# Performance work log

Hardware: AMD Instinct MI355X
Metric: run time of the kernel (lower is better)

The kernel has to match this reference:

```python
import jax, jax.numpy as jnp
import numpy as np

D_MODEL = 1024
D_STATE = 128
D_CONV = 4
EXPAND = 2
HEADDIM = 64
D_INNER = EXPAND * D_MODEL          # 2048
NHEADS = D_INNER // HEADDIM         # 32
NGROUPS = 1
CONV_DIM = D_INNER + 2 * NGROUPS * D_STATE            # 2304
D_IN_PROJ = 2 * D_INNER + 2 * NGROUPS * D_STATE + NHEADS  # 4384
NUM_CLASS = 48
BATCH = 2
SEQLEN = 512


def setup_inputs() -> dict:
    key = jax.random.key(0)
    ks = jax.random.split(key, 8)
    s = 0.02
    inputs = jax.random.normal(ks[0], (BATCH, SEQLEN, D_MODEL), jnp.float32)
    W_in = jax.random.normal(ks[1], (D_MODEL, D_IN_PROJ), jnp.float32) * s
    conv_w = jax.random.normal(ks[2], (CONV_DIM, D_CONV), jnp.float32) * 0.2
    conv_b = jnp.zeros((CONV_DIM,), jnp.float32)
    # dt_bias = inverse-softplus of dt sampled in [1e-3, 0.1] (mamba init)
    dt = jnp.exp(jax.random.uniform(ks[3], (NHEADS,), jnp.float32) * (np.log(0.1) - np.log(1e-3)) + np.log(1e-3))
    dt_bias = dt + jnp.log(-jnp.expm1(-dt))
    A_log = jnp.log(jax.random.uniform(ks[4], (NHEADS,), jnp.float32, 1.0, 16.0))
    D = jnp.ones((NHEADS,), jnp.float32)
    norm_w = jnp.ones((D_INNER,), jnp.float32)
    W_out = jax.random.normal(ks[5], (D_INNER, D_MODEL), jnp.float32) * s
    W_cls = jax.random.normal(ks[6], (D_INNER, NUM_CLASS), jnp.float32) * s
    b_cls = jnp.zeros((NUM_CLASS,), jnp.float32)
    return {"inputs": inputs, "W_in": W_in, "conv_w": conv_w, "conv_b": conv_b,
            "dt_bias": dt_bias, "A_log": A_log, "D": D, "norm_w": norm_w,
            "W_out": W_out, "W_cls": W_cls, "b_cls": b_cls}


def _forward(inputs, W_in, conv_w, conv_b, dt_bias, A_log, D, norm_w, W_out, W_cls, b_cls):
    B, L, _ = inputs.shape
    zxbcdt = inputs @ W_in                                     # (B,L,4384)
    z, xBC, dt = jnp.split(zxbcdt, [D_INNER, D_INNER + CONV_DIM], axis=-1)
    dt = jax.nn.softplus(dt + dt_bias)                         # (B,L,H)
    # causal depthwise conv over time on (x,B,C)
    xBC_t = jnp.pad(jnp.transpose(xBC, (0, 2, 1)), ((0, 0), (0, 0), (D_CONV - 1, 0)))
    xBC_c = jax.lax.conv_general_dilated(xBC_t, conv_w[:, None, :], (1,), 'VALID',
                                         feature_group_count=CONV_DIM)
    xBC = jax.nn.silu(jnp.transpose(xBC_c, (0, 2, 1)) + conv_b)
    x, Bm, Cm = jnp.split(xBC, [D_INNER, D_INNER + D_STATE], axis=-1)
    x = x.reshape(B, L, NHEADS, HEADDIM)
    A = -jnp.exp(A_log)                                        # (H,)
    dA = jnp.exp(dt * A)                                       # (B,L,H)

    def step(state, inp):
        # state: (B,H,P,N) -- selective SSM recurrence (chunk_size=1 path)
        x_t, B_t, C_t, dt_t, dA_t = inp
        state = state * dA_t[:, :, None, None] + jnp.einsum('bhp,bn,bh->bhpn', x_t, B_t, dt_t)
        y_t = jnp.einsum('bhpn,bn->bhp', state, C_t)
        return state, y_t

    state0 = jnp.zeros((B, NHEADS, HEADDIM, D_STATE), inputs.dtype)
    xs = (jnp.transpose(x, (1, 0, 2, 3)), jnp.transpose(Bm, (1, 0, 2)),
          jnp.transpose(Cm, (1, 0, 2)), jnp.transpose(dt, (1, 0, 2)),
          jnp.transpose(dA, (1, 0, 2)))
    _, ys = jax.lax.scan(step, state0, xs)                     # ys: (L,B,H,P)
    y = jnp.transpose(ys, (1, 0, 2, 3)) + D[None, None, :, None] * x
    y = y.reshape(B, L, D_INNER)
    # gated RMSNorm: rmsnorm(y * silu(z)) * weight
    y = y * jax.nn.silu(z)
    y = y * jax.lax.rsqrt(jnp.mean(y * y, axis=-1, keepdims=True) + 1e-5) * norm_w
    # hidden_states (d_inner=2048) go through the per-timestep classifier
    preds = y @ W_cls + b_cls                                  # (B,L,num_class)
    return preds


def reference(inputs, W_in, conv_w, conv_b, dt_bias, A_log, D, norm_w, W_out, W_cls, b_cls):
    return _forward(inputs, W_in, conv_w, conv_b, dt_bias, A_log, D, norm_w, W_out, W_cls, b_cls)
```

## Files before the change

kernel.cpp:

```cpp
#include <hip/hip_runtime.h>
#include <hip/hip_bf16.h>
#include <cstdint>

#define BATCH 2
#define SEQLEN 512
#define BL (BATCH*SEQLEN)
#define DMODEL 1024
#define DINNER 2048
#define NHEADS 32
#define HEADDIM 64
#define DSTATE 128
#define CONVDIM 2304
#define DINPROJ 4384
#define NPROJPAD 4480
#define NCLS 48
#define QC 64
#define NCH 8

typedef short bf16x8 __attribute__((ext_vector_type(8)));
typedef float f32x4  __attribute__((ext_vector_type(4)));
typedef unsigned int u32;
typedef const __attribute__((address_space(1))) u32 gu32;
typedef __attribute__((address_space(3))) u32 lu32;

static __device__ __forceinline__ void gl16(const void* g, void* l) {
    __builtin_amdgcn_global_load_lds((gu32*)g, (lu32*)l, 16, 0, 0);
}

static __device__ __forceinline__ unsigned short f2bf(float f) {
    unsigned u = __float_as_uint(f);
    unsigned r = (u + 0x7FFFu + ((u >> 16) & 1u)) >> 16;
    return (unsigned short)r;
}
static __device__ __forceinline__ float bf2f(unsigned short u) {
    return __uint_as_float(((unsigned)u) << 16);
}

__global__ __launch_bounds__(256) void k_prep(const float* __restrict__ in,
                                              unsigned short* __restrict__ abf,
                                              const float* __restrict__ W,
                                              unsigned short* __restrict__ Wt,
                                              const float* __restrict__ Wcls,
                                              unsigned short* __restrict__ Wtc) {
    __shared__ float tile[32][33];
    int bid = blockIdx.x;
    int tid = threadIdx.x;
    if (bid < 1024) {
        int i = (bid * 256 + tid) * 4;
        float4 v = *(const float4*)(in + i);
        ushort4 o;
        o.x = f2bf(v.x); o.y = f2bf(v.y); o.z = f2bf(v.z); o.w = f2bf(v.w);
        *(ushort4*)(abf + i) = o;
    } else if (bid < 1024 + 4384) {
        int t = bid - 1024;
        int n0 = (t % 137) * 32;
        int k0 = (t / 137) * 32;
        int tx = tid & 31, ty = tid >> 5;
#pragma unroll
        for (int i = 0; i < 4; ++i) {
            int k = k0 + ty + i * 8;
            tile[ty + i * 8][tx] = W[(size_t)k * DINPROJ + n0 + tx];
        }
        __syncthreads();
#pragma unroll
        for (int i = 0; i < 4; ++i) {
            int n = n0 + ty + i * 8;
            Wt[(size_t)n * DMODEL + k0 + tx] = f2bf(tile[tx][ty + i * 8]);
        }
    } else {
        int n = bid - (1024 + 4384);
        for (int k = tid; k < DINNER; k += 256)
            Wtc[(size_t)n * DINNER + k] = f2bf(Wcls[(size_t)k * NCLS + n]);
    }
}

__global__ __launch_bounds__(256) void k_gemm_in(const unsigned short* __restrict__ A,
                                                 const unsigned short* __restrict__ Bt,
                                                 unsigned short* __restrict__ C) {
    __shared__ unsigned short As[2 * 4096];
    __shared__ unsigned short Bs[2 * 5120];
    const int tid  = threadIdx.x;
    const int m0   = blockIdx.y * 128;
    const int n0   = blockIdx.x * 160;
    const int w    = tid >> 6;
    const int lane = tid & 63;
    const int wm   = w >> 1, wn = w & 1;
    const int fr   = lane & 15, fq = lane >> 4;
    const int lrow = lane >> 2;
    const int skg  = (lane & 3) * 8;
    const unsigned short* gA0 = A + (size_t)(m0 + w * 16 + lrow) * DMODEL + skg;
    const unsigned short* gA1 = gA0 + (size_t)64 * DMODEL;

    f32x4 acc[4][5] = {};
    for (int k0 = 0; k0 < DMODEL; k0 += 64) {
        __syncthreads();
#pragma unroll
        for (int hh = 0; hh < 2; ++hh) {
            int kg = k0 + hh * 32;
            gl16(gA0 + kg, As + hh * 4096 + w * 512);
            gl16(gA1 + kg, As + hh * 4096 + 2048 + w * 512);
            for (int o = w; o < 10; o += 4) {
                const unsigned short* gB = Bt + (size_t)(n0 + o * 16 + lrow) * DMODEL + skg + kg;
                gl16(gB, Bs + hh * 5120 + o * 512);
            }
        }
        __syncthreads();
#pragma unroll
        for (int hh = 0; hh < 2; ++hh) {
            bf16x8 af[4], bfr[5];
#pragma unroll
            for (int mt = 0; mt < 4; ++mt)
                af[mt] = *(const bf16x8*)(&As[hh * 4096 + (wm * 64 + mt * 16 + fr) * 32 + fq * 8]);
#pragma unroll
            for (int nt = 0; nt < 5; ++nt)
                bfr[nt] = *(const bf16x8*)(&Bs[hh * 5120 + (wn * 80 + nt * 16 + fr) * 32 + fq * 8]);
#pragma unroll
            for (int mt = 0; mt < 4; ++mt)
#pragma unroll
                for (int nt = 0; nt < 5; ++nt)
                    acc[mt][nt] = __builtin_amdgcn_mfma_f32_16x16x32_bf16(af[mt], bfr[nt], acc[mt][nt], 0, 0, 0);
        }
    }
#pragma unroll
    for (int mt = 0; mt < 4; ++mt) {
#pragma unroll
        for (int nt = 0; nt < 5; ++nt) {
            int col = n0 + wn * 80 + nt * 16 + fr;
            if (col < DINPROJ) {
#pragma unroll
                for (int r = 0; r < 4; ++r) {
                    int row = m0 + wm * 64 + mt * 16 + fq * 4 + r;
                    C[(size_t)row * DINPROJ + col] = f2bf(acc[mt][nt][r]);
                }
            }
        }
    }
}

__global__ __launch_bounds__(256) void k_conv_dt(const unsigned short* __restrict__ zx,
                                                 const float* __restrict__ conv_w,
                                                 const float* __restrict__ conv_b,
                                                 const float* __restrict__ dt_bias,
                                                 float* __restrict__ xbc,
                                                 float* __restrict__ dtb) {
    int row = blockIdx.y;
    int c   = blockIdx.x * 256 + threadIdx.x;
    int b = row >> 9, l = row & 511;
    if (c < CONVDIM) {
        float acc = conv_b[c];
#pragma unroll
        for (int j = 0; j < 4; ++j) {
            int ls = l - 3 + j;
            float v = (ls >= 0) ? bf2f(zx[((size_t)(b * SEQLEN + ls)) * DINPROJ + DINNER + c]) : 0.f;
            acc += v * conv_w[c * 4 + j];
        }
        float s = acc / (1.f + expf(-acc));
        xbc[(size_t)row * CONVDIM + c] = s;
    } else if (c < CONVDIM + NHEADS) {
        int h = c - CONVDIM;
        float raw = bf2f(zx[(size_t)row * DINPROJ + (DINNER + CONVDIM) + h]) + dt_bias[h];
        float dt = (raw > 20.f) ? raw : log1pf(expf(raw));
        dtb[row * NHEADS + h] = dt;
    }
}

__global__ __launch_bounds__(256) void k_chunk(const float* __restrict__ xbc,
                                               const float* __restrict__ dtb,
                                               const float* __restrict__ A_log,
                                               const float* __restrict__ Dvec,
                                               unsigned short* __restrict__ yb,
                                               unsigned short* __restrict__ Sc_bf,
                                               float* __restrict__ lam_g,
                                               float* __restrict__ esc_g) {
    const int gid = blockIdx.x;
    const int cq = gid & 7;
    const int h = (gid >> 3) & 31;
    const int b = gid >> 8;
    const int row0 = b * SEQLEN + cq * QC;

    __shared__ float cumS[QC], wS[QC], dtS[QC];
    __shared__ unsigned short Xt[QC][72];
    __shared__ unsigned short Bs[QC][136];
    __shared__ unsigned short BtW[DSTATE][72];
    __shared__ unsigned short Cs[QC][136];
    __shared__ unsigned short Gs[QC][72];

    const int tid = threadIdx.x;
    if (tid < 64) {
        float dtv = dtb[(size_t)(row0 + tid) * NHEADS + h];
        float nA = -expf(A_log[h]);
        float x = dtv * nA;
#pragma unroll
        for (int off = 1; off < 64; off <<= 1) {
            float v = __shfl_up(x, off, 64);
            if (tid >= off) x += v;
        }
        float cumTot = __shfl(x, 63, 64);
        cumS[tid] = x;
        dtS[tid] = dtv;
        wS[tid] = expf(cumTot - x) * dtv;
        esc_g[(size_t)gid * QC + tid] = expf(x);
        if (tid == 0) lam_g[gid] = expf(cumTot);
    }
    __syncthreads();

    {
        int row = tid >> 2;
        int g = tid & 3;
        const float* rp = xbc + (size_t)(row0 + row) * CONVDIM;
        float wrow = wS[row];
#pragma unroll
        for (int i = 0; i < 4; ++i) {
            float4 v = *(const float4*)(rp + h * HEADDIM + g * 16 + i * 4);
            int p = g * 16 + i * 4;
            Xt[p + 0][row] = f2bf(v.x);
            Xt[p + 1][row] = f2bf(v.y);
            Xt[p + 2][row] = f2bf(v.z);
            Xt[p + 3][row] = f2bf(v.w);
        }
#pragma unroll
        for (int i = 0; i < 8; ++i) {
            int n = g * 32 + i * 4;
            float4 v = *(const float4*)(rp + DINNER + n);
            ushort4 u;
            u.x = f2bf(v.x); u.y = f2bf(v.y); u.z = f2bf(v.z); u.w = f2bf(v.w);
            *(ushort4*)(&Bs[row][n]) = u;
            BtW[n + 0][row] = f2bf(v.x * wrow);
            BtW[n + 1][row] = f2bf(v.y * wrow);
            BtW[n + 2][row] = f2bf(v.z * wrow);
            BtW[n + 3][row] = f2bf(v.w * wrow);
        }
#pragma unroll
        for (int i = 0; i < 8; ++i) {
            int n = g * 32 + i * 4;
            float4 v = *(const float4*)(rp + DINNER + DSTATE + n);
            ushort4 u;
            u.x = f2bf(v.x); u.y = f2bf(v.y); u.z = f2bf(v.z); u.w = f2bf(v.w);
            *(ushort4*)(&Cs[row][n]) = u;
        }
    }
    __syncthreads();

    const int w = tid >> 6, lane = tid & 63;
    const int fr = lane & 15, fq = lane >> 4, fk = (lane >> 4) * 8;

    f32x4 accG[4] = {};
#pragma unroll
    for (int kk = 0; kk < 4; ++kk) {
        bf16x8 a = *(const bf16x8*)(&Cs[w * 16 + fr][kk * 32 + fk]);
#pragma unroll
        for (int nt = 0; nt < 4; ++nt) {
            bf16x8 bb = *(const bf16x8*)(&Bs[nt * 16 + fr][kk * 32 + fk]);
            accG[nt] = __builtin_amdgcn_mfma_f32_16x16x32_bf16(a, bb, accG[nt], 0, 0, 0);
        }
    }
#pragma unroll
    for (int nt = 0; nt < 4; ++nt) {
        int s = nt * 16 + fr;
        float cs = cumS[s], dts = dtS[s];
#pragma unroll
        for (int r = 0; r < 4; ++r) {
            int t = w * 16 + fq * 4 + r;
            float val = (s <= t) ? accG[nt][r] * expf(cumS[t] - cs) * dts : 0.f;
            Gs[t][s] = f2bf(val);
        }
    }
    __syncthreads();

    f32x4 accY[4] = {};
#pragma unroll
    for (int kk = 0; kk < 2; ++kk) {
        bf16x8 a = *(const bf16x8*)(&Gs[w * 16 + fr][kk * 32 + fk]);
#pragma unroll
        for (int pt = 0; pt < 4; ++pt) {
            bf16x8 bb = *(const bf16x8*)(&Xt[pt * 16 + fr][kk * 32 + fk]);
            accY[pt] = __builtin_amdgcn_mfma_f32_16x16x32_bf16(a, bb, accY[pt], 0, 0, 0);
        }
    }
    f32x4 accS[8] = {};
#pragma unroll
    for (int kk = 0; kk < 2; ++kk) {
        bf16x8 a = *(const bf16x8*)(&Xt[w * 16 + fr][kk * 32 + fk]);
#pragma unroll
        for (int nt = 0; nt < 8; ++nt) {
            bf16x8 bb = *(const bf16x8*)(&BtW[nt * 16 + fr][kk * 32 + fk]);
            accS[nt] = __builtin_amdgcn_mfma_f32_16x16x32_bf16(a, bb, accS[nt], 0, 0, 0);
        }
    }
    float Dh = Dvec[h];
#pragma unroll
    for (int pt = 0; pt < 4; ++pt) {
        int p = pt * 16 + fr;
#pragma unroll
        for (int r = 0; r < 4; ++r) {
            int t = w * 16 + fq * 4 + r;
            float xv = bf2f(Xt[p][t]);
            yb[(size_t)(row0 + t) * DINNER + h * HEADDIM + p] = f2bf(accY[pt][r] + Dh * xv);
        }
    }
    unsigned short* scp = Sc_bf + (size_t)gid * (HEADDIM * DSTATE);
#pragma unroll
    for (int nt = 0; nt < 8; ++nt) {
        int n = nt * 16 + fr;
#pragma unroll
        for (int r = 0; r < 4; ++r) {
            int p = w * 16 + fq * 4 + r;
            scp[p * DSTATE + n] = f2bf(accS[nt][r]);
        }
    }
}

__global__ __launch_bounds__(256) void k_cross(const float* __restrict__ xbc,
                                               const float* __restrict__ esc_g,
                                               const unsigned short* __restrict__ Sc_bf,
                                               const float* __restrict__ lam_g,
                                               unsigned short* __restrict__ yb) {
    const int gid = blockIdx.x;
    const int cq = gid & 7;
    if (cq == 0) return;
    const int h = (gid >> 3) & 31;
    const int b = gid >> 8;
    const int row0 = b * SEQLEN + cq * QC;
    __shared__ unsigned short Ct[QC][136];
    __shared__ unsigned short Ss[QC][136];
    const int tid = threadIdx.x;
    const int gbase = gid & ~7;

    float coef[NCH - 1];
    {
        float prod = 1.f;
        for (int c2 = cq - 1; c2 >= 0; --c2) {
            coef[c2] = prod;
            prod *= lam_g[gbase + c2];
        }
    }
    {
        int row = tid >> 2, g = tid & 3;
        const float* rp = xbc + (size_t)(row0 + row) * CONVDIM + DINNER + DSTATE;
        float esc = esc_g[(size_t)gid * QC + row];
#pragma unroll
        for (int i = 0; i < 8; ++i) {
            int n = g * 32 + i * 4;
            float4 v = *(const float4*)(rp + n);
            ushort4 u;
            u.x = f2bf(v.x * esc); u.y = f2bf(v.y * esc);
            u.z = f2bf(v.z * esc); u.w = f2bf(v.w * esc);
            *(ushort4*)(&Ct[row][n]) = u;
        }
        float acc32[32];
#pragma unroll
        for (int i = 0; i < 32; ++i) acc32[i] = 0.f;
        for (int c2 = 0; c2 < cq; ++c2) {
            const unsigned short* sp = Sc_bf + (size_t)(gbase + c2) * (HEADDIM * DSTATE)
                                     + row * DSTATE + g * 32;
            float cf = coef[c2];
#pragma unroll
            for (int i = 0; i < 8; ++i) {
                ushort4 v = *(const ushort4*)(sp + i * 4);
                acc32[i * 4 + 0] += cf * bf2f(v.x);
                acc32[i * 4 + 1] += cf * bf2f(v.y);
                acc32[i * 4 + 2] += cf * bf2f(v.z);
                acc32[i * 4 + 3] += cf * bf2f(v.w);
            }
        }
#pragma unroll
        for (int i = 0; i < 8; ++i) {
            ushort4 u;
            u.x = f2bf(acc32[i * 4 + 0]);
            u.y = f2bf(acc32[i * 4 + 1]);
            u.z = f2bf(acc32[i * 4 + 2]);
            u.w = f2bf(acc32[i * 4 + 3]);
            *(ushort4*)(&Ss[row][g * 32 + i * 4]) = u;
        }
    }
    __syncthreads();
    const int w = tid >> 6, lane = tid & 63;
    const int fr = lane & 15, fq = lane >> 4, fk = (lane >> 4) * 8;
    f32x4 acc[4] = {};
#pragma unroll
    for (int kk = 0; kk < 4; ++kk) {
        bf16x8 a = *(const bf16x8*)(&Ct[w * 16 + fr][kk * 32 + fk]);
#pragma unroll
        for (int pt = 0; pt < 4; ++pt) {
            bf16x8 bb = *(const bf16x8*)(&Ss[pt * 16 + fr][kk * 32 + fk]);
            acc[pt] = __builtin_amdgcn_mfma_f32_16x16x32_bf16(a, bb, acc[pt], 0, 0, 0);
        }
    }
#pragma unroll
    for (int pt = 0; pt < 4; ++pt) {
        int p = pt * 16 + fr;
#pragma unroll
        for (int r = 0; r < 4; ++r) {
            int t = w * 16 + fq * 4 + r;
            size_t yi = (size_t)(row0 + t) * DINNER + h * HEADDIM + p;
            yb[yi] = f2bf(bf2f(yb[yi]) + acc[pt][r]);
        }
    }
}

__global__ __launch_bounds__(256) void k_gn_cls(const unsigned short* __restrict__ zx,
                                                const unsigned short* __restrict__ yb,
                                                const float* __restrict__ nw,
                                                const unsigned short* __restrict__ Wt,
                                                const float* __restrict__ bcls,
                                                float* __restrict__ out) {
    __shared__ unsigned short Gs[16][2048];
    __shared__ float scaleS[16];
    __shared__ float Rs[3][4][256];
    const int m0 = blockIdx.x * 16;
    const int tid = threadIdx.x;
    const int w = tid >> 6, lane = tid & 63;

#pragma unroll
    for (int i = 0; i < 4; ++i) {
        int rl = w * 4 + i;
        int row = m0 + rl;
        const unsigned short* yr = yb + (size_t)row * DINNER;
        const unsigned short* zr = zx + (size_t)row * DINPROJ;
        float gv[32];
        float ss = 0.f;
#pragma unroll
        for (int i2 = 0; i2 < 4; ++i2) {
            int k = i2 * 512 + lane * 8;
            ushort4 ya = *(const ushort4*)(yr + k);
            ushort4 ybq = *(const ushort4*)(yr + k + 4);
            ushort4 za = *(const ushort4*)(zr + k);
            ushort4 zbq = *(const ushort4*)(zr + k + 4);
            float ys[8] = {bf2f(ya.x), bf2f(ya.y), bf2f(ya.z), bf2f(ya.w),
                           bf2f(ybq.x), bf2f(ybq.y), bf2f(ybq.z), bf2f(ybq.w)};
            float zs[8] = {bf2f(za.x), bf2f(za.y), bf2f(za.z), bf2f(za.w),
                           bf2f(zbq.x), bf2f(zbq.y), bf2f(zbq.z), bf2f(zbq.w)};
#pragma unroll
            for (int j = 0; j < 8; ++j) {
                float sil = zs[j] / (1.f + expf(-zs[j]));
                float gg = ys[j] * sil;
                gv[i2 * 8 + j] = gg;
                ss += gg * gg;
            }
        }
#pragma unroll
        for (int off = 32; off >= 1; off >>= 1) ss += __shfl_xor(ss, off, 64);
        if (lane == 0) scaleS[rl] = rsqrtf(ss / (float)DINNER + 1e-5f);
#pragma unroll
        for (int i2 = 0; i2 < 4; ++i2) {
            int k = i2 * 512 + lane * 8;
            ushort4 u0, u1;
            u0.x = f2bf(gv[i2 * 8 + 0]); u0.y = f2bf(gv[i2 * 8 + 1]);
            u0.z = f2bf(gv[i2 * 8 + 2]); u0.w = f2bf(gv[i2 * 8 + 3]);
            u1.x = f2bf(gv[i2 * 8 + 4]); u1.y = f2bf(gv[i2 * 8 + 5]);
            u1.z = f2bf(gv[i2 * 8 + 6]); u1.w = f2bf(gv[i2 * 8 + 7]);
            *(ushort4*)(&Gs[rl][k]) = u0;
            *(ushort4*)(&Gs[rl][k + 4]) = u1;
        }
    }
    __syncthreads();
    {
        int k0 = tid * 8;
        float4 n0 = *(const float4*)(nw + k0);
        float4 n1 = *(const float4*)(nw + k0 + 4);
        float nv[8] = {n0.x, n0.y, n0.z, n0.w, n1.x, n1.y, n1.z, n1.w};
#pragma unroll
        for (int r = 0; r < 16; ++r) {
            float sc = scaleS[r];
            ushort4 a0 = *(const ushort4*)(&Gs[r][k0]);
            ushort4 a1 = *(const ushort4*)(&Gs[r][k0 + 4]);
            ushort4 o0, o1;
            o0.x = f2bf(bf2f(a0.x) * sc * nv[0]); o0.y = f2bf(bf2f(a0.y) * sc * nv[1]);
            o0.z = f2bf(bf2f(a0.z) * sc * nv[2]); o0.w = f2bf(bf2f(a0.w) * sc * nv[3]);
            o1.x = f2bf(bf2f(a1.x) * sc * nv[4]); o1.y = f2bf(bf2f(a1.y) * sc * nv[5]);
            o1.z = f2bf(bf2f(a1.z) * sc * nv[6]); o1.w = f2bf(bf2f(a1.w) * sc * nv[7]);
            *(ushort4*)(&Gs[r][k0]) = o0;
            *(ushort4*)(&Gs[r][k0 + 4]) = o1;
        }
    }
    __syncthreads();
    const int fr = lane & 15, fq = lane >> 4;
    f32x4 acc[3] = {};
    const int kbase = w * 512;
    for (int ks = 0; ks < 16; ++ks) {
        int k0 = kbase + ks * 32;
        bf16x8 a = *(const bf16x8*)(&Gs[fr][k0 + fq * 8]);
#pragma unroll
        for (int nt = 0; nt < 3; ++nt) {
            bf16x8 bb = *(const bf16x8*)(Wt + (size_t)(nt * 16 + fr) * DINNER + k0 + fq * 8);
            acc[nt] = __builtin_amdgcn_mfma_f32_16x16x32_bf16(a, bb, acc[nt], 0, 0, 0);
        }
    }
#pragma unroll
    for (int nt = 0; nt < 3; ++nt)
        *(f32x4*)(&Rs[nt][w][lane * 4]) = acc[nt];
    __syncthreads();
    if (tid < 64) {
#pragma unroll
        for (int nt = 0; nt < 3; ++nt) {
            int col = nt * 16 + (lane & 15);
            float bb = bcls[col];
#pragma unroll
            for (int j = 0; j < 4; ++j) {
                float s = Rs[nt][0][lane * 4 + j] + Rs[nt][1][lane * 4 + j]
                        + Rs[nt][2][lane * 4 + j] + Rs[nt][3][lane * 4 + j];
                int row = m0 + (lane >> 4) * 4 + j;
                out[(size_t)row * NCLS + col] = s + bb;
            }
        }
    }
}

extern "C" void kernel_launch(void* const* d_in, const int* in_sizes, int n_in,
                              void* d_out, int out_size, void* d_ws, size_t ws_size,
                              hipStream_t stream) {
    const float* inputs  = (const float*)d_in[0];
    const float* W_in    = (const float*)d_in[1];
    const float* conv_w  = (const float*)d_in[2];
    const float* conv_b  = (const float*)d_in[3];
    const float* dt_bias = (const float*)d_in[4];
    const float* A_log   = (const float*)d_in[5];
    const float* Dvec    = (const float*)d_in[6];
    const float* norm_w  = (const float*)d_in[7];
    const float* W_cls   = (const float*)d_in[9];
    const float* b_cls   = (const float*)d_in[10];
    float* out = (float*)d_out;

    float* ws = (float*)d_ws;
    unsigned short* zxb = (unsigned short*)ws;
    float* xbc   = ws + (size_t)BL * DINPROJ / 2;
    float* dtb   = xbc + (size_t)BL * CONVDIM;
    float* lam_g = dtb + (size_t)BL * NHEADS;
    float* esc_g = lam_g + 512;
    unsigned short* yb     = (unsigned short*)(esc_g + 512 * QC);
    unsigned short* Sc_bf  = yb + (size_t)BL * DINNER;
    unsigned short* abf    = Sc_bf + (size_t)512 * HEADDIM * DSTATE;
    unsigned short* wtbf   = abf + (size_t)BL * DMODEL;
    unsigned short* wclsbf = wtbf + (size_t)NPROJPAD * DMODEL;

    k_prep<<<dim3(1024 + 4384 + 48), dim3(256), 0, stream>>>(inputs, abf, W_in, wtbf,
                                                             W_cls, wclsbf);
    k_gemm_in<<<dim3(NPROJPAD / 160, BL / 128), dim3(256), 0, stream>>>(abf, wtbf, zxb);
    k_conv_dt<<<dim3(10, BL), dim3(256), 0, stream>>>(zxb, conv_w, conv_b, dt_bias, xbc, dtb);
    k_chunk<<<dim3(BATCH * NHEADS * NCH), dim3(256), 0, stream>>>(xbc, dtb, A_log, Dvec,
                                                                  yb, Sc_bf, lam_g, esc_g);
    k_cross<<<dim3(BATCH * NHEADS * NCH), dim3(256), 0, stream>>>(xbc, esc_g, Sc_bf,
                                                                  lam_g, yb);
    k_gn_cls<<<dim3(BL / 16), dim3(256), 0, stream>>>(zxb, yb, norm_w, wclsbf, b_cls, out);
}
```

Measured before the change: 174.7 us.

## Fuse causal conv, SiLU and dt softplus into chunk and cross kernels

Removes the separate conv/dt kernel and its fp32 xbc/dtb intermediates. k_chunk now computes the depthwise causal conv plus SiLU for its head's x slice and for B and C directly from the bf16 projection output, and computes softplus(dt) inline. k_cross recomputes the conv for C, scaled by the per-row decay loaded into shared memory. This saves one launch and a large fp32 write and read round trip. The cost is redundant conv work: every head block recomputes B and C, and k_cross recomputes C again.

```diff
diff --git a/kernel.cpp b/kernel.cpp
--- a/kernel.cpp
+++ b/kernel.cpp
@@ -137,35 +137,10 @@
     }
 }
 
-__global__ __launch_bounds__(256) void k_conv_dt(const unsigned short* __restrict__ zx,
-                                                 const float* __restrict__ conv_w,
-                                                 const float* __restrict__ conv_b,
-                                                 const float* __restrict__ dt_bias,
-                                                 float* __restrict__ xbc,
-                                                 float* __restrict__ dtb) {
-    int row = blockIdx.y;
-    int c   = blockIdx.x * 256 + threadIdx.x;
-    int b = row >> 9, l = row & 511;
-    if (c < CONVDIM) {
-        float acc = conv_b[c];
-#pragma unroll
-        for (int j = 0; j < 4; ++j) {
-            int ls = l - 3 + j;
-            float v = (ls >= 0) ? bf2f(zx[((size_t)(b * SEQLEN + ls)) * DINPROJ + DINNER + c]) : 0.f;
-            acc += v * conv_w[c * 4 + j];
-        }
-        float s = acc / (1.f + expf(-acc));
-        xbc[(size_t)row * CONVDIM + c] = s;
-    } else if (c < CONVDIM + NHEADS) {
-        int h = c - CONVDIM;
-        float raw = bf2f(zx[(size_t)row * DINPROJ + (DINNER + CONVDIM) + h]) + dt_bias[h];
-        float dt = (raw > 20.f) ? raw : log1pf(expf(raw));
-        dtb[row * NHEADS + h] = dt;
-    }
-}
-
-__global__ __launch_bounds__(256) void k_chunk(const float* __restrict__ xbc,
-                                               const float* __restrict__ dtb,
+__global__ __launch_bounds__(256) void k_chunk(const unsigned short* __restrict__ zx,
+                                               const float* __restrict__ conv_w,
+                                               const float* __restrict__ conv_b,
+                                               const float* __restrict__ dt_bias,
                                                const float* __restrict__ A_log,
                                                const float* __restrict__ Dvec,
                                                unsigned short* __restrict__ yb,
@@ -187,7 +162,8 @@
 
     const int tid = threadIdx.x;
     if (tid < 64) {
-        float dtv = dtb[(size_t)(row0 + tid) * NHEADS + h];
+        float raw = bf2f(zx[(size_t)(row0 + tid) * DINPROJ + (DINNER + CONVDIM) + h]) + dt_bias[h];
+        float dtv = (raw > 20.f) ? raw : log1pf(expf(raw));
         float nA = -expf(A_log[h]);
         float x = dtv * nA;
 #pragma unroll
@@ -205,38 +181,58 @@
     __syncthreads();
 
     {
-        int row = tid >> 2;
-        int g = tid & 3;
-        const float* rp = xbc + (size_t)(row0 + row) * CONVDIM;
-        float wrow = wS[row];
-#pragma unroll
-        for (int i = 0; i < 4; ++i) {
-            float4 v = *(const float4*)(rp + h * HEADDIM + g * 16 + i * 4);
-            int p = g * 16 + i * 4;
-            Xt[p + 0][row] = f2bf(v.x);
-            Xt[p + 1][row] = f2bf(v.y);
-            Xt[p + 2][row] = f2bf(v.z);
-            Xt[p + 3][row] = f2bf(v.w);
-        }
-#pragma unroll
-        for (int i = 0; i < 8; ++i) {
-            int n = g * 32 + i * 4;
-            float4 v = *(const float4*)(rp + DINNER + n);
-            ushort4 u;
-            u.x = f2bf(v.x); u.y = f2bf(v.y); u.z = f2bf(v.z); u.w = f2bf(v.w);
-            *(ushort4*)(&Bs[row][n]) = u;
-            BtW[n + 0][row] = f2bf(v.x * wrow);
-            BtW[n + 1][row] = f2bf(v.y * wrow);
-            BtW[n + 2][row] = f2bf(v.z * wrow);
-            BtW[n + 3][row] = f2bf(v.w * wrow);
-        }
-#pragma unroll
-        for (int i = 0; i < 8; ++i) {
-            int n = g * 32 + i * 4;
-            float4 v = *(const float4*)(rp + DINNER + DSTATE + n);
-            ushort4 u;
-            u.x = f2bf(v.x); u.y = f2bf(v.y); u.z = f2bf(v.z); u.w = f2bf(v.w);
-            *(ushort4*)(&Cs[row][n]) = u;
+        const unsigned short* zbase = zx + (size_t)b * SEQLEN * DINPROJ + DINNER;
+        const int l0 = cq * QC;
+        for (int it = 0; it < 20; ++it) {
+            int work = it * 256 + tid;
+            int r = work / 80;
+            int cc = work - r * 80;
+            int ch;
+            if (cc < 16)      ch = h * 64 + cc * 4;
+            else if (cc < 48) ch = 2048 + (cc - 16) * 4;
+            else              ch = 2176 + (cc - 48) * 4;
+            float fi[4][4];
+#pragma unroll
+            for (int j = 0; j < 4; ++j) {
+                int l = l0 + r - 3 + j;
+                if (l >= 0) {
+                    ushort4 v = *(const ushort4*)(zbase + (size_t)l * DINPROJ + ch);
+                    fi[j][0] = bf2f(v.x); fi[j][1] = bf2f(v.y);
+                    fi[j][2] = bf2f(v.z); fi[j][3] = bf2f(v.w);
+                } else {
+                    fi[j][0] = fi[j][1] = fi[j][2] = fi[j][3] = 0.f;
+                }
+            }
+            float o[4];
+#pragma unroll
+            for (int c = 0; c < 4; ++c) {
+                float4 cw = *(const float4*)(conv_w + (size_t)(ch + c) * 4);
+                float a = conv_b[ch + c] + cw.x * fi[0][c] + cw.y * fi[1][c]
+                        + cw.z * fi[2][c] + cw.w * fi[3][c];
+                o[c] = a / (1.f + expf(-a));
+            }
+            if (cc < 16) {
+                int p = cc * 4;
+                Xt[p + 0][r] = f2bf(o[0]);
+                Xt[p + 1][r] = f2bf(o[1]);
+                Xt[p + 2][r] = f2bf(o[2]);
+                Xt[p + 3][r] = f2bf(o[3]);
+            } else if (cc < 48) {
+                int n = (cc - 16) * 4;
+                ushort4 u;
+                u.x = f2bf(o[0]); u.y = f2bf(o[1]); u.z = f2bf(o[2]); u.w = f2bf(o[3]);
+                *(ushort4*)(&Bs[r][n]) = u;
+                float wrow = wS[r];
+                BtW[n + 0][r] = f2bf(o[0] * wrow);
+                BtW[n + 1][r] = f2bf(o[1] * wrow);
+                BtW[n + 2][r] = f2bf(o[2] * wrow);
+                BtW[n + 3][r] = f2bf(o[3] * wrow);
+            } else {
+                int n = (cc - 48) * 4;
+                ushort4 u;
+                u.x = f2bf(o[0]); u.y = f2bf(o[1]); u.z = f2bf(o[2]); u.w = f2bf(o[3]);
+                *(ushort4*)(&Cs[r][n]) = u;
+            }
         }
     }
     __syncthreads();
@@ -310,7 +306,9 @@
     }
 }
 
-__global__ __launch_bounds__(256) void k_cross(const float* __restrict__ xbc,
+__global__ __launch_bounds__(256) void k_cross(const unsigned short* __restrict__ zx,
+                                               const float* __restrict__ conv_w,
+                                               const float* __restrict__ conv_b,
                                                const float* __restrict__ esc_g,
                                                const unsigned short* __restrict__ Sc_bf,
                                                const float* __restrict__ lam_g,
@@ -323,8 +321,11 @@
     const int row0 = b * SEQLEN + cq * QC;
     __shared__ unsigned short Ct[QC][136];
     __shared__ unsigned short Ss[QC][136];
+    __shared__ float escS[QC];
     const int tid = threadIdx.x;
     const int gbase = gid & ~7;
+
+    if (tid < 64) escS[tid] = esc_g[(size_t)gid * QC + tid];
 
     float coef[NCH - 1];
     {
@@ -336,17 +337,6 @@
     }
     {
         int row = tid >> 2, g = tid & 3;
-        const float* rp = xbc + (size_t)(row0 + row) * CONVDIM + DINNER + DSTATE;
-        float esc = esc_g[(size_t)gid * QC + row];
-#pragma unroll
-        for (int i = 0; i < 8; ++i) {
-            int n = g * 32 + i * 4;
-            float4 v = *(const float4*)(rp + n);
-            ushort4 u;
-            u.x = f2bf(v.x * esc); u.y = f2bf(v.y * esc);
-            u.z = f2bf(v.z * esc); u.w = f2bf(v.w * esc);
-            *(ushort4*)(&Ct[row][n]) = u;
-        }
         float acc32[32];
 #pragma unroll
         for (int i = 0; i < 32; ++i) acc32[i] = 0.f;
@@ -371,6 +361,37 @@
             u.z = f2bf(acc32[i * 4 + 2]);
             u.w = f2bf(acc32[i * 4 + 3]);
             *(ushort4*)(&Ss[row][g * 32 + i * 4]) = u;
+        }
+    }
+    __syncthreads();
+    {
+        const unsigned short* zbase = zx + (size_t)b * SEQLEN * DINPROJ + DINNER;
+        const int l0 = cq * QC;
+        for (int it = 0; it < 8; ++it) {
+            int work = it * 256 + tid;
+            int r = work >> 5;
+            int n = (work & 31) * 4;
+            int ch = 2176 + n;
+            float fi[4][4];
+#pragma unroll
+            for (int j = 0; j < 4; ++j) {
+                int l = l0 + r - 3 + j;
+                ushort4 v = *(const ushort4*)(zbase + (size_t)l * DINPROJ + ch);
+                fi[j][0] = bf2f(v.x); fi[j][1] = bf2f(v.y);
+                fi[j][2] = bf2f(v.z); fi[j][3] = bf2f(v.w);
+            }
+            float esc = escS[r];
+            ushort4 u;
+            float o[4];
+#pragma unroll
+            for (int c = 0; c < 4; ++c) {
+                float4 cw = *(const float4*)(conv_w + (size_t)(ch + c) * 4);
+                float a = conv_b[ch + c] + cw.x * fi[0][c] + cw.y * fi[1][c]
+                        + cw.z * fi[2][c] + cw.w * fi[3][c];
+                o[c] = (a / (1.f + expf(-a))) * esc;
+            }
+            u.x = f2bf(o[0]); u.y = f2bf(o[1]); u.z = f2bf(o[2]); u.w = f2bf(o[3]);
+            *(ushort4*)(&Ct[r][n]) = u;
         }
     }
     __syncthreads();
@@ -523,9 +544,7 @@
 
     float* ws = (float*)d_ws;
     unsigned short* zxb = (unsigned short*)ws;
-    float* xbc   = ws + (size_t)BL * DINPROJ / 2;
-    float* dtb   = xbc + (size_t)BL * CONVDIM;
-    float* lam_g = dtb + (size_t)BL * NHEADS;
+    float* lam_g = ws + (size_t)BL * DINPROJ / 2;
     float* esc_g = lam_g + 512;
     unsigned short* yb     = (unsigned short*)(esc_g + 512 * QC);
     unsigned short* Sc_bf  = yb + (size_t)BL * DINNER;
@@ -536,10 +555,10 @@
     k_prep<<<dim3(1024 + 4384 + 48), dim3(256), 0, stream>>>(inputs, abf, W_in, wtbf,
                                                              W_cls, wclsbf);
     k_gemm_in<<<dim3(NPROJPAD / 160, BL / 128), dim3(256), 0, stream>>>(abf, wtbf, zxb);
-    k_conv_dt<<<dim3(10, BL), dim3(256), 0, stream>>>(zxb, conv_w, conv_b, dt_bias, xbc, dtb);
-    k_chunk<<<dim3(BATCH * NHEADS * NCH), dim3(256), 0, stream>>>(xbc, dtb, A_log, Dvec,
+    k_chunk<<<dim3(BATCH * NHEADS * NCH), dim3(256), 0, stream>>>(zxb, conv_w, conv_b,
+                                                                  dt_bias, A_log, Dvec,
                                                                   yb, Sc_bf, lam_g, esc_g);
-    k_cross<<<dim3(BATCH * NHEADS * NCH), dim3(256), 0, stream>>>(xbc, esc_g, Sc_bf,
-                                                                  lam_g, yb);
+    k_cross<<<dim3(BATCH * NHEADS * NCH), dim3(256), 0, stream>>>(zxb, conv_w, conv_b,
+                                                                  esc_g, Sc_bf, lam_g, yb);
     k_gn_cls<<<dim3(BL / 16), dim3(256), 0, stream>>>(zxb, yb, norm_w, wclsbf, b_cls, out);
 }
```

Result: slower. 193.2 us (+10.6%).
